# Optimization experiments

Hardware: AMD Instinct MI355X
Metric: run time of the kernel (lower is better)

The kernel has to match this reference:

```python
import jax, jax.numpy as jnp
import numpy as np

ALPHA = 0.2  # LeakyReLU negative slope
NEG_INF = -9e15  # matches torch's -9000000000000000.0


def setup_inputs() -> dict:
    key = jax.random.key(0)
    k1, k2, k3, k4 = jax.random.split(key, 4)
    B, T, N, F_in, D = 4, 32, 512, 128, 128
    h = jax.random.normal(k1, (B, T, N, F_in), dtype=jnp.float32)
    adj = jax.random.randint(k2, (N, N), 0, 2, dtype=jnp.int32)
    # params: W ~ Linear(in_dim, out_dim, bias=False); a ~ Linear(2*out_dim, 1, bias=False)
    W = jax.random.normal(k3, (F_in, D), dtype=jnp.float32) * 0.05
    a = jax.random.normal(k4, (2 * D,), dtype=jnp.float32) * 0.05
    return {"h": h, "adj": adj, "W": W, "a": a}


def reference(h, adj, W, a):
    # h: (B,T,N,F_in), adj: (N,N), W: (F_in,D), a: (2D,)
    D = W.shape[1]
    Wh = jnp.einsum('btnf,fd->btnd', h, W)  # (B,T,N,D)
    # a . [Wh_i ; Wh_j] == a_src . Wh_i + a_dst . Wh_j -- avoids (N,N,2D) concat
    a_src, a_dst = a[:D], a[D:]
    e_src = Wh @ a_src  # (B,T,N)
    e_dst = Wh @ a_dst  # (B,T,N)
    e = jax.nn.leaky_relu(e_src[..., :, None] + e_dst[..., None, :], ALPHA)  # (B,T,N,N)
    e = jnp.where(adj > 0, e, jnp.float32(NEG_INF))
    attention = jax.nn.softmax(e, axis=-1)  # dropout is identity at eval
    h_prime = jnp.einsum('btij,btjd->btid', attention, Wh)  # (B,T,N,D)
    return h_prime
```

## Files before the change

kernel.cpp:

```cpp
#include <hip/hip_runtime.h>
#include <math.h>

typedef __attribute__((ext_vector_type(8))) short bf16x8;
typedef __attribute__((ext_vector_type(4))) float f32x4;

#define MFMA(a, b, c) __builtin_amdgcn_mfma_f32_16x16x32_bf16(a, b, c, 0, 0, 0)

constexpr int GN = 128;
constexpr int NN = 512;
constexpr int FD = 128;
#define LOG2E 1.4426950408889634f

__device__ inline unsigned rne_top16(float x) {
    unsigned u = __float_as_uint(x);
    return u + 0x7fffu + ((u >> 16) & 1u);
}
__device__ inline unsigned pack_top16(unsigned e1, unsigned e0) {
    return __builtin_amdgcn_perm(e1, e0, 0x07060302u);
}
__device__ inline void gload16(const void* g, void* l) {
    __builtin_amdgcn_global_load_lds(
        (const __attribute__((address_space(1))) unsigned*)g,
        (__attribute__((address_space(3))) unsigned*)l, 16, 0, 0);
}

__global__ __launch_bounds__(256, 2) void whb_kernel(
    const float* __restrict__ h, const float* __restrict__ a,
    const int* __restrict__ adj, const float* __restrict__ W,
    unsigned short* __restrict__ whtHi,
    float* __restrict__ esrc, float* __restrict__ edst,
    unsigned* __restrict__ mask)
{
    __shared__ __attribute__((aligned(16))) unsigned short sW[32768];

    const int bid = blockIdx.x;
    const int xcd = bid & 7, slot = bid >> 3;
    const int g = xcd + 8 * (slot >> 2);
    const int jt = slot & 3;
    const int t = threadIdx.x, lane = t & 63, w = t >> 6;
    const int i0r = jt * 128;
    const int q8 = (lane >> 4) * 8;
    const float* hg = h + (size_t)(g * NN) * FD;

    float4 hv[16];
    #pragma unroll
    for (int kk = 0; kk < 4; ++kk)
        #pragma unroll
        for (int mt = 0; mt < 2; ++mt) {
            const float* src = hg + (size_t)(i0r + w * 32 + mt * 16 + (lane & 15)) * FD
                             + kk * 32 + q8;
            hv[(kk * 2 + mt) * 2 + 0] = *(const float4*)src;
            hv[(kk * 2 + mt) * 2 + 1] = *(const float4*)(src + 4);
        }

    {
        const int pred0 = adj[bid * NN + t] > 0;
        const int pred1 = adj[bid * NN + 256 + t] > 0;
        const unsigned long long m0 = __ballot(pred0);
        const unsigned long long m1 = __ballot(pred1);
        if (lane == 0) {
            mask[bid * 16 + 2 * w]     = (unsigned)m0;
            mask[bid * 16 + 8 + 2 * w] = (unsigned)m1;
        } else if (lane == 1) {
            mask[bid * 16 + 2 * w + 1]     = (unsigned)(m0 >> 32);
            mask[bid * 16 + 8 + 2 * w + 1] = (unsigned)(m1 >> 32);
        }
    }

    #pragma unroll
    for (int grp = 0; grp < 8; ++grp) {
        const int p8 = grp * 256 + t;
        const int lanep = p8 & 63, cn = p8 >> 6;
        const int kks = cn >> 3, nbs = cn & 7;
        const int kbase = kks * 32 + ((lanep >> 4) & 3) * 8;
        const int d = nbs * 16 + (lanep & 15);
        unsigned hi[8], lo[8];
        #pragma unroll
        for (int idx = 0; idx < 8; ++idx) {
            const float wv = W[(kbase + idx) * FD + d];
            const unsigned u = __float_as_uint(wv);
            hi[idx] = u;
            lo[idx] = rne_top16(wv - __uint_as_float(u & 0xffff0000u));
        }
        uint4 H4, L4;
        H4.x = pack_top16(hi[1], hi[0]); H4.y = pack_top16(hi[3], hi[2]);
        H4.z = pack_top16(hi[5], hi[4]); H4.w = pack_top16(hi[7], hi[6]);
        L4.x = pack_top16(lo[1], lo[0]); L4.y = pack_top16(lo[3], lo[2]);
        L4.z = pack_top16(lo[5], lo[4]); L4.w = pack_top16(lo[7], lo[6]);
        *(uint4*)&sW[p8 * 8]         = H4;
        *(uint4*)&sW[16384 + p8 * 8] = L4;
    }
    __syncthreads();

    f32x4 acc[2][8];
    #pragma unroll
    for (int mt = 0; mt < 2; ++mt)
        #pragma unroll
        for (int nb = 0; nb < 8; ++nb) acc[mt][nb] = (f32x4){0.f, 0.f, 0.f, 0.f};

    #pragma unroll
    for (int kk = 0; kk < 4; ++kk) {
        bf16x8 ah[2], al[2];
        #pragma unroll
        for (int mt = 0; mt < 2; ++mt) {
            const float4 f0 = hv[(kk * 2 + mt) * 2 + 0];
            const float4 f1 = hv[(kk * 2 + mt) * 2 + 1];
            const float xs[8] = {f0.x, f0.y, f0.z, f0.w, f1.x, f1.y, f1.z, f1.w};
            union { bf16x8 v; unsigned u[4]; } H, L;
            #pragma unroll
            for (int j = 0; j < 4; ++j) {
                const unsigned e0 = __float_as_uint(xs[2 * j]);
                const unsigned e1 = __float_as_uint(xs[2 * j + 1]);
                H.u[j] = pack_top16(e1, e0);
                const unsigned l0 = rne_top16(xs[2*j]   - __uint_as_float(e0 & 0xffff0000u));
                const unsigned l1 = rne_top16(xs[2*j+1] - __uint_as_float(e1 & 0xffff0000u));
                L.u[j] = pack_top16(l1, l0);
            }
            ah[mt] = H.v; al[mt] = L.v;
        }
        #pragma unroll
        for (int nb = 0; nb < 8; ++nb) {
            const bf16x8 bh = *(const bf16x8*)&sW[((kk * 8 + nb) * 64 + lane) * 8];
            const bf16x8 bl = *(const bf16x8*)&sW[16384 + ((kk * 8 + nb) * 64 + lane) * 8];
            #pragma unroll
            for (int mt = 0; mt < 2; ++mt) {
                acc[mt][nb] = MFMA(al[mt], bh, acc[mt][nb]);
                acc[mt][nb] = MFMA(ah[mt], bl, acc[mt][nb]);
                acc[mt][nb] = MFMA(ah[mt], bh, acc[mt][nb]);
            }
        }
    }

    float av[8], bv[8];
    #pragma unroll
    for (int nb = 0; nb < 8; ++nb) {
        av[nb] = a[nb * 16 + (lane & 15)];
        bv[nb] = a[FD + nb * 16 + (lane & 15)];
    }
    #pragma unroll
    for (int mt = 0; mt < 2; ++mt)
        #pragma unroll
        for (int r = 0; r < 4; ++r) {
            float ps = 0.f, pd = 0.f;
            #pragma unroll
            for (int nb = 0; nb < 8; ++nb) {
                ps += acc[mt][nb][r] * av[nb];
                pd += acc[mt][nb][r] * bv[nb];
            }
            #pragma unroll
            for (int off = 1; off <= 8; off <<= 1) {
                ps += __shfl_xor(ps, off);
                pd += __shfl_xor(pd, off);
            }
            if ((lane & 15) == 0) {
                const int row = g * NN + i0r + w * 32 + mt * 16 + (lane >> 4) * 4 + r;
                esrc[row] = ps;
                edst[row] = pd;
            }
        }

    unsigned short* sT = sW;
    const size_t gbase = (size_t)g * 65536 + (size_t)jt * 16384;
    const int ib = 4 * ((lane >> 4) & 1);

    __syncthreads();
    #pragma unroll
    for (int mt = 0; mt < 2; ++mt) {
        const int lp2 = (lane & 15) + 16 * (mt * 2 + (lane >> 5));
        #pragma unroll
        for (int nb = 0; nb < 8; ++nb) {
            const int off = ((w * 8 + nb) * 64 + lp2) * 8 + ib;
            const unsigned r0 = rne_top16(acc[mt][nb][0]);
            const unsigned r1 = rne_top16(acc[mt][nb][1]);
            const unsigned r2 = rne_top16(acc[mt][nb][2]);
            const unsigned r3 = rne_top16(acc[mt][nb][3]);
            *(uint2*)&sT[off] = make_uint2(pack_top16(r1, r0), pack_top16(r3, r2));
        }
    }
    __syncthreads();
    for (int q = t; q < 2048; q += 256)
        *(float4*)&whtHi[gbase + q * 8] = *(const float4*)&sT[q * 8];
}

__global__ __launch_bounds__(256, 2) void attn_kernel(
    const unsigned short* __restrict__ whtHi,
    const float* __restrict__ esrc, const float* __restrict__ edst,
    const unsigned* __restrict__ mask, float* __restrict__ out)
{
    __shared__ __attribute__((aligned(16))) unsigned short cHi[2][16384];
    __shared__ __attribute__((aligned(16))) float eds[NN];
    __shared__ unsigned maskS[128 * 17];

    const int bid = blockIdx.x;
    const int xcd = bid & 7, slot = bid >> 3;
    const int g = xcd + 8 * (slot >> 2);
    const int it = slot & 3;
    const int t = threadIdx.x, lane = t & 63, w = t >> 6;
    const int i0 = it * 128;
    const int q8 = (lane >> 4) * 8;
    const int l15 = lane & 15;

    const size_t gbase = (size_t)g * 65536;
    for (int q = t; q < 2048; q += 256)
        gload16(&whtHi[gbase + q * 8], &cHi[0][q * 8]);

    eds[t]       = edst[g * NN + t] * LOG2E;
    eds[t + 256] = edst[g * NN + 256 + t] * LOG2E;
    for (int q = t; q < 2048; q += 256) {
        const int row = q >> 4, wo = q & 15;
        maskS[row * 17 + wo] = mask[(i0 + row) * 16 + wo];
    }

    const int rloc0 = w * 32 + l15;
    const int rloc1 = rloc0 + 16;
    const float s0 = esrc[g * NN + i0 + rloc0] * LOG2E;
    const float s1 = esrc[g * NN + i0 + rloc1] * LOG2E;

    union { bf16x8 v; unsigned short s[8]; } bo;
    {
        const unsigned short oneb = (l15 == 0) ? (unsigned short)0x3f80 : (unsigned short)0;
        #pragma unroll
        for (int j = 0; j < 8; ++j) bo.s[j] = oneb;
    }

    __syncthreads();

    f32x4 acc[2][8];
    #pragma unroll
    for (int mt = 0; mt < 2; ++mt)
        #pragma unroll
        for (int nb = 0; nb < 8; ++nb) acc[mt][nb] = (f32x4){0.f, 0.f, 0.f, 0.f};
    f32x4 accS0 = (f32x4){0.f, 0.f, 0.f, 0.f};
    f32x4 accS1 = (f32x4){0.f, 0.f, 0.f, 0.f};

    for (int c4 = 0; c4 < 4; ++c4) {
        const int cur = c4 & 1, nxt = cur ^ 1;
        if (c4 < 3) {
            const size_t gb = gbase + (size_t)(c4 + 1) * 16384;
            for (int q = t; q < 2048; q += 256)
                gload16(&whtHi[gb + q * 8], &cHi[nxt][q * 8]);
        }
        const unsigned short* __restrict__ bHi = &cHi[cur][0];
        #pragma unroll
        for (int kl = 0; kl < 4; ++kl) {
            const int KK = c4 * 4 + kl;
            const float* ep = &eds[KK * 32 + q8];
            const float4 ed0 = *(const float4*)ep;
            const float4 ed1 = *(const float4*)(ep + 4);
            const float ev[8] = {ed0.x, ed0.y, ed0.z, ed0.w, ed1.x, ed1.y, ed1.z, ed1.w};
            const unsigned mw0 = maskS[rloc0 * 17 + KK] >> q8;
            const unsigned mw1 = maskS[rloc1 * 17 + KK] >> q8;

            union { bf16x8 v; unsigned u[4]; } H0, H1;
            unsigned uh0[8], uh1[8];
            #pragma unroll
            for (int i = 0; i < 8; ++i) {
                const float z0 = s0 + ev[i];
                float p0 = __builtin_amdgcn_exp2f(fmaxf(z0, 0.2f * z0));
                p0 = ((mw0 >> i) & 1u) ? p0 : 0.f;
                uh0[i] = __float_as_uint(p0);
                const float z1 = s1 + ev[i];
                float p1 = __builtin_amdgcn_exp2f(fmaxf(z1, 0.2f * z1));
                p1 = ((mw1 >> i) & 1u) ? p1 : 0.f;
                uh1[i] = __float_as_uint(p1);
            }
            #pragma unroll
            for (int j = 0; j < 4; ++j) {
                H0.u[j] = pack_top16(uh0[2*j+1], uh0[2*j]);
                H1.u[j] = pack_top16(uh1[2*j+1], uh1[2*j]);
            }
            #pragma unroll
            for (int nb = 0; nb < 8; ++nb) {
                const bf16x8 bh = *(const bf16x8*)&bHi[((kl * 8 + nb) * 64 + lane) * 8];
                acc[0][nb] = MFMA(H0.v, bh, acc[0][nb]);
                acc[1][nb] = MFMA(H1.v, bh, acc[1][nb]);
            }
            accS0 = MFMA(H0.v, bo.v, accS0);
            accS1 = MFMA(H1.v, bo.v, accS1);
        }
        __syncthreads();
    }

    #pragma unroll
    for (int r = 0; r < 4; ++r) {
        const float rl0 = 1.0f / __shfl(accS0[r], lane & 48);
        const float rl1 = 1.0f / __shfl(accS1[r], lane & 48);
        const int row0 = g * NN + i0 + w * 32 + (lane >> 4) * 4 + r;
        const int row1 = row0 + 16;
        #pragma unroll
        for (int nb = 0; nb < 8; ++nb) {
            out[row0 * FD + nb * 16 + l15] = acc[0][nb][r] * rl0;
            out[row1 * FD + nb * 16 + l15] = acc[1][nb][r] * rl1;
        }
    }
}

extern "C" void kernel_launch(void* const* d_in, const int* in_sizes, int n_in,
                              void* d_out, int out_size, void* d_ws, size_t ws_size,
                              hipStream_t stream) {
    const float* h   = (const float*)d_in[0];
    const int*   adj = (const int*)d_in[1];
    const float* W   = (const float*)d_in[2];
    const float* a   = (const float*)d_in[3];
    float* out = (float*)d_out;

    unsigned short* whtHi = (unsigned short*)d_ws;
    float* esrc = (float*)(whtHi + (size_t)GN * 65536);
    float* edst = esrc + GN * NN;
    unsigned* mask = (unsigned*)(edst + GN * NN);

    whb_kernel<<<512, 256, 0, stream>>>(h, a, adj, W, whtHi, esrc, edst, mask);
    attn_kernel<<<512, 256, 0, stream>>>(whtHi, esrc, edst, mask, out);
}
```

Measured before the change: 112.4 us.

## Stage intermediates in output buffer and build adjacency mask inside attention kernel

Intermediate bf16 Wh, e_src and e_dst now live in each group's slice of the output buffer instead of a separate workspace. The four attention blocks of a group coordinate with an atomic counter so no block overwrites that slice before all of them have finished reading it. The adjacency bitmask is now built inside the attention kernel from adj, which removes the separate mask write and read but has every block repeat the mask build. The change adds a spin-wait that depends on co-residency and gives up after a retry cap, so correctness rests on scheduling assumptions.

```diff
diff --git a/kernel.cpp b/kernel.cpp
--- a/kernel.cpp
+++ b/kernel.cpp
@@ -24,12 +24,10 @@
         (__attribute__((address_space(3))) unsigned*)l, 16, 0, 0);
 }
 
+
 __global__ __launch_bounds__(256, 2) void whb_kernel(
     const float* __restrict__ h, const float* __restrict__ a,
-    const int* __restrict__ adj, const float* __restrict__ W,
-    unsigned short* __restrict__ whtHi,
-    float* __restrict__ esrc, float* __restrict__ edst,
-    unsigned* __restrict__ mask)
+    const float* __restrict__ W, float* __restrict__ outF)
 {
     __shared__ __attribute__((aligned(16))) unsigned short sW[32768];
 
@@ -42,6 +40,15 @@
     const int q8 = (lane >> 4) * 8;
     const float* hg = h + (size_t)(g * NN) * FD;
 
+    float* reg = outF + (size_t)g * 65536;
+    unsigned short* whtg = (unsigned short*)reg;
+    float* esrcg = reg + 32768;
+    float* edstg = reg + 33280;
+
+    if (jt == 0 && t == 0)
+        __hip_atomic_store((unsigned*)(reg + 33792), 0u,
+                           __ATOMIC_RELAXED, __HIP_MEMORY_SCOPE_AGENT);
+
     float4 hv[16];
     #pragma unroll
     for (int kk = 0; kk < 4; ++kk)
@@ -52,20 +59,6 @@
             hv[(kk * 2 + mt) * 2 + 0] = *(const float4*)src;
             hv[(kk * 2 + mt) * 2 + 1] = *(const float4*)(src + 4);
         }
-
-    {
-        const int pred0 = adj[bid * NN + t] > 0;
-        const int pred1 = adj[bid * NN + 256 + t] > 0;
-        const unsigned long long m0 = __ballot(pred0);
-        const unsigned long long m1 = __ballot(pred1);
-        if (lane == 0) {
-            mask[bid * 16 + 2 * w]     = (unsigned)m0;
-            mask[bid * 16 + 8 + 2 * w] = (unsigned)m1;
-        } else if (lane == 1) {
-            mask[bid * 16 + 2 * w + 1]     = (unsigned)(m0 >> 32);
-            mask[bid * 16 + 8 + 2 * w + 1] = (unsigned)(m1 >> 32);
-        }
-    }
 
     #pragma unroll
     for (int grp = 0; grp < 8; ++grp) {
@@ -153,14 +146,13 @@
                 pd += __shfl_xor(pd, off);
             }
             if ((lane & 15) == 0) {
-                const int row = g * NN + i0r + w * 32 + mt * 16 + (lane >> 4) * 4 + r;
-                esrc[row] = ps;
-                edst[row] = pd;
+                const int rowl = i0r + w * 32 + mt * 16 + (lane >> 4) * 4 + r;
+                esrcg[rowl] = ps;
+                edstg[rowl] = pd;
             }
         }
 
     unsigned short* sT = sW;
-    const size_t gbase = (size_t)g * 65536 + (size_t)jt * 16384;
     const int ib = 4 * ((lane >> 4) & 1);
 
     __syncthreads();
@@ -178,14 +170,13 @@
         }
     }
     __syncthreads();
+    const int sbase = jt * 16384;
     for (int q = t; q < 2048; q += 256)
-        *(float4*)&whtHi[gbase + q * 8] = *(const float4*)&sT[q * 8];
+        *(float4*)&whtg[sbase + q * 8] = *(const float4*)&sT[q * 8];
 }
 
 __global__ __launch_bounds__(256, 2) void attn_kernel(
-    const unsigned short* __restrict__ whtHi,
-    const float* __restrict__ esrc, const float* __restrict__ edst,
-    const unsigned* __restrict__ mask, float* __restrict__ out)
+    const int* __restrict__ adj, float* __restrict__ outF)
 {
     __shared__ __attribute__((aligned(16))) unsigned short cHi[2][16384];
     __shared__ __attribute__((aligned(16))) float eds[NN];
@@ -200,21 +191,36 @@
     const int q8 = (lane >> 4) * 8;
     const int l15 = lane & 15;
 
-    const size_t gbase = (size_t)g * 65536;
+    float* reg = outF + (size_t)g * 65536;
+    const unsigned short* whtg = (const unsigned short*)reg;
+    const float* esrcg = reg + 32768;
+    const float* edstg = reg + 33280;
+    unsigned* cnt = (unsigned*)(reg + 33792);
+
     for (int q = t; q < 2048; q += 256)
-        gload16(&whtHi[gbase + q * 8], &cHi[0][q * 8]);
-
-    eds[t]       = edst[g * NN + t] * LOG2E;
-    eds[t + 256] = edst[g * NN + 256 + t] * LOG2E;
+        gload16(&whtg[q * 8], &cHi[0][q * 8]);
+
+    eds[t]       = edstg[t] * LOG2E;
+    eds[t + 256] = edstg[t + 256] * LOG2E;
     for (int q = t; q < 2048; q += 256) {
         const int row = q >> 4, wo = q & 15;
-        maskS[row * 17 + wo] = mask[(i0 + row) * 16 + wo];
+        const int* p = adj + (size_t)(i0 + row) * NN + wo * 32;
+        unsigned m = 0;
+        #pragma unroll
+        for (int b = 0; b < 32; b += 4) {
+            const int4 v = *(const int4*)&p[b];
+            m |= (v.x > 0 ? 1u : 0u) << b;
+            m |= (v.y > 0 ? 1u : 0u) << (b + 1);
+            m |= (v.z > 0 ? 1u : 0u) << (b + 2);
+            m |= (v.w > 0 ? 1u : 0u) << (b + 3);
+        }
+        maskS[row * 17 + wo] = m;
     }
 
     const int rloc0 = w * 32 + l15;
     const int rloc1 = rloc0 + 16;
-    const float s0 = esrc[g * NN + i0 + rloc0] * LOG2E;
-    const float s1 = esrc[g * NN + i0 + rloc1] * LOG2E;
+    const float s0 = esrcg[i0 + rloc0] * LOG2E;
+    const float s1 = esrcg[i0 + rloc1] * LOG2E;
 
     union { bf16x8 v; unsigned short s[8]; } bo;
     {
@@ -236,9 +242,9 @@
     for (int c4 = 0; c4 < 4; ++c4) {
         const int cur = c4 & 1, nxt = cur ^ 1;
         if (c4 < 3) {
-            const size_t gb = gbase + (size_t)(c4 + 1) * 16384;
+            const int sb = (c4 + 1) * 16384;
             for (int q = t; q < 2048; q += 256)
-                gload16(&whtHi[gb + q * 8], &cHi[nxt][q * 8]);
+                gload16(&whtg[sb + q * 8], &cHi[nxt][q * 8]);
         }
         const unsigned short* __restrict__ bHi = &cHi[cur][0];
         #pragma unroll
@@ -279,7 +285,19 @@
             accS1 = MFMA(H1.v, bo.v, accS1);
         }
         __syncthreads();
-    }
+        if (c4 == 2 && t == 0)
+            __hip_atomic_fetch_add(cnt, 1u, __ATOMIC_RELAXED,
+                                   __HIP_MEMORY_SCOPE_AGENT);
+    }
+
+    if (it != 3 && t == 0) {
+        int tries = 0;
+        while (__hip_atomic_load(cnt, __ATOMIC_RELAXED,
+                                 __HIP_MEMORY_SCOPE_AGENT) < 4u
+               && ++tries < 100000)
+            __builtin_amdgcn_s_sleep(8);
+    }
+    __syncthreads();
 
     #pragma unroll
     for (int r = 0; r < 4; ++r) {
@@ -289,8 +307,8 @@
         const int row1 = row0 + 16;
         #pragma unroll
         for (int nb = 0; nb < 8; ++nb) {
-            out[row0 * FD + nb * 16 + l15] = acc[0][nb][r] * rl0;
-            out[row1 * FD + nb * 16 + l15] = acc[1][nb][r] * rl1;
+            outF[row0 * FD + nb * 16 + l15] = acc[0][nb][r] * rl0;
+            outF[row1 * FD + nb * 16 + l15] = acc[1][nb][r] * rl1;
         }
     }
 }
@@ -303,12 +321,8 @@
     const float* W   = (const float*)d_in[2];
     const float* a   = (const float*)d_in[3];
     float* out = (float*)d_out;
-
-    unsigned short* whtHi = (unsigned short*)d_ws;
-    float* esrc = (float*)(whtHi + (size_t)GN * 65536);
-    float* edst = esrc + GN * NN;
-    unsigned* mask = (unsigned*)(edst + GN * NN);
-
-    whb_kernel<<<512, 256, 0, stream>>>(h, a, adj, W, whtHi, esrc, edst, mask);
-    attn_kernel<<<512, 256, 0, stream>>>(whtHi, esrc, edst, mask, out);
-}
+    (void)d_ws; (void)ws_size;
+
+    whb_kernel<<<512, 256, 0, stream>>>(h, a, W, out);
+    attn_kernel<<<512, 256, 0, stream>>>(adj, out);
+}
```

Measured after the change: 126.5 us. 1.13x slower.
